# Kernel optimization log

Measured on AMD Instinct MI355X. Metric: run time of the kernel, lower is better.

## Reference

```python
import jax, jax.numpy as jnp
import numpy as np

N_OBJ = 8        # objects per sample -> nc2 = 28 pair-nodes per sample (code caps nc2 < 30)
MAX_REL = 10     # relations per sample (num_rel is uniform so total_rels is static)


def setup_inputs() -> dict:
    key = jax.random.key(0)
    k1, k2, k3, k4, k5 = jax.random.split(key, 5)
    B, D, n = 1024, 512, N_OBJ
    iu, ju = np.triu_indices(n, k=1)                     # (i<j) pair layout, lexicographic
    nc2 = iu.shape[0]                                     # 28
    bcol = np.repeat(np.arange(B), nc2)
    slicing_tensor = jnp.asarray(
        np.stack([bcol, np.tile(iu, B), np.tile(ju, B)], axis=1), dtype=jnp.int32)  # [B*nc2, 3]
    spatial_branch_feature_map = jax.random.normal(k1, (B * nc2, D), dtype=jnp.float32)
    W_self = jax.random.normal(k2, (D, D), dtype=jnp.float32) / np.float32(np.sqrt(D))
    W_nbr = jax.random.normal(k3, (D, D), dtype=jnp.float32) / np.float32(np.sqrt(D))
    b = jnp.zeros((D,), dtype=jnp.float32)
    # object_pairs: distinct indices in [0, n)
    i0 = jax.random.randint(k4, (B, MAX_REL), 0, n)
    off = jax.random.randint(k5, (B, MAX_REL), 1, n)
    i1 = (i0 + off) % n
    object_pairs = jnp.stack([i0, i1], axis=-1).astype(jnp.int32)  # [B, MAX_REL, 2]
    num_rel = jnp.full((B,), MAX_REL, dtype=jnp.int32)
    num_obj = jnp.full((B,), n, dtype=jnp.int32)
    return {"spatial_branch_feature_map": spatial_branch_feature_map, "W_self": W_self,
            "W_nbr": W_nbr, "b": b, "slicing_tensor": slicing_tensor,
            "object_pairs": object_pairs, "num_rel": num_rel, "num_obj": num_obj}


def reference(spatial_branch_feature_map, W_self, W_nbr, b,
              slicing_tensor, object_pairs, num_rel, num_obj):
    x = spatial_branch_feature_map
    N, D = x.shape
    B = num_obj.shape[0]
    nc2 = N // B                                          # pair-nodes per sample
    n = N_OBJ
    # --- fully-connected edge index per sample (incl. self-loops), offset per batch ---
    src_l = jnp.repeat(jnp.arange(nc2, dtype=jnp.int32), nc2)   # row0: t1 outer loop
    dst_l = jnp.tile(jnp.arange(nc2, dtype=jnp.int32), nc2)     # row1: t2 inner loop
    offs = (jnp.arange(B, dtype=jnp.int32) * nc2)[:, None]
    src = (src_l[None, :] + offs).reshape(-1)                   # [B*nc2^2]
    dst = (dst_l[None, :] + offs).reshape(-1)
    # --- GNN layer: sum-aggregate neighbor messages, linear + ReLU ---
    agg = jax.ops.segment_sum(x[src], dst, num_segments=N)      # [N, D]
    h = jax.nn.relu(x @ W_self + agg @ W_nbr + b)               # [N, D]
    # --- key-matching gather (replaces nested python-loop boolean matching) ---
    keys = slicing_tensor[:, 0] * (n * n) + slicing_tensor[:, 1] * n + slicing_tensor[:, 2]
    lut = jnp.zeros((B * n * n,), dtype=jnp.int32).at[keys].set(jnp.arange(N, dtype=jnp.int32))
    pmin = jnp.minimum(object_pairs[..., 0], object_pairs[..., 1])
    pmax = jnp.maximum(object_pairs[..., 0], object_pairs[..., 1])
    bidx = jnp.arange(B, dtype=jnp.int32)[:, None]
    rel_keys = (bidx * (n * n) + pmin * n + pmax).reshape(-1)   # [B*MAX_REL]
    rows = lut[rel_keys]
    return h[rows]                                              # [total_rels, D]
```

## Files before the change

### kernel.cpp

```cpp
#include <hip/hip_runtime.h>
#include <hip/hip_bf16.h>
#include <stdint.h>


typedef __bf16 bf16_t;
typedef __bf16 bf16x8 __attribute__((ext_vector_type(8)));
typedef __bf16 bf16x4 __attribute__((ext_vector_type(4)));
typedef float  f32x4  __attribute__((ext_vector_type(4)));

#define D_DIM 512
#define NC2   28
#define NOBJ  8
#define MAXREL 10
#define B_SAMP 1024
#define OUTROWS (B_SAMP * MAXREL)

__device__ __forceinline__ void gload_lds16(const void* g, void* l) {
  __builtin_amdgcn_global_load_lds(
      (const __attribute__((address_space(1))) unsigned int*)g,
      (__attribute__((address_space(3))) unsigned int*)l, 16, 0, 0);
}

__global__ __launch_bounds__(256) void prep_kernel(
    const float* __restrict__ x, const float* __restrict__ Wself,
    const float* __restrict__ Wnbr, const int* __restrict__ pairs,
    bf16_t* __restrict__ Sbf, bf16_t* __restrict__ Abf,
    bf16_t* __restrict__ Wst, bf16_t* __restrict__ Wnt)
{
  const int blk = blockIdx.x, tid = threadIdx.x;
  if (blk < B_SAMP) {
    __shared__ int rel_row[MAXREL];
    __shared__ float4 oddsum[128];
    if (tid < MAXREL) {
      int p0 = pairs[blk * MAXREL * 2 + tid * 2 + 0];
      int p1 = pairs[blk * MAXREL * 2 + tid * 2 + 1];
      int pmin = min(p0, p1), pmax = max(p0, p1);
      rel_row[tid] = 7 * pmin - (pmin * (pmin - 1)) / 2 + (pmax - pmin - 1);
    }
    __syncthreads();

    const int h = tid >> 7, c = tid & 127;
    const float4* x4 = (const float4*)(x + (size_t)blk * NC2 * D_DIM);
    float4 a = {0.f, 0.f, 0.f, 0.f};
    #pragma unroll
    for (int rp = 0; rp < NC2 / 2; ++rp) {
      float4 v = x4[(rp * 2 + h) * 128 + c];
      a.x += v.x; a.y += v.y; a.z += v.z; a.w += v.w;
    }
    if (h) oddsum[c] = a;
    __syncthreads();
    if (!h) {
      float4 b = oddsum[c];
      bf16x4 o = { (bf16_t)(a.x + b.x), (bf16_t)(a.y + b.y),
                   (bf16_t)(a.z + b.z), (bf16_t)(a.w + b.w) };
      *(bf16x4*)(Sbf + (size_t)blk * D_DIM + c * 4) = o;
    }
    #pragma unroll
    for (int j = h; j < MAXREL; j += 2) {
      float4 v = x4[rel_row[j] * 128 + c];
      bf16x4 o = { (bf16_t)v.x, (bf16_t)v.y, (bf16_t)v.z, (bf16_t)v.w };
      *(bf16x4*)(Abf + (size_t)(blk * MAXREL + j) * D_DIM + c * 4) = o;
    }
  } else {
    __shared__ float tile[32][33];
    const int t = blk - B_SAMP;
    const float* W  = (t & 256) ? Wnbr : Wself;
    bf16_t*     Wt  = (t & 256) ? Wnt  : Wst;
    const int r = t & 255;
    const int k0 = (r & 15) * 32, n0 = (r >> 4) * 32;
    const int tx = tid & 31, ty = tid >> 5;
    #pragma unroll
    for (int i = 0; i < 32; i += 8)
      tile[ty + i][tx] = W[(size_t)(k0 + ty + i) * D_DIM + n0 + tx];
    __syncthreads();
    #pragma unroll
    for (int i = 0; i < 32; i += 8)
      Wt[(size_t)(n0 + ty + i) * D_DIM + k0 + tx] = (bf16_t)tile[tx][ty + i];
  }
}

#define SA_BYTES 6144
#define SB_BYTES 8192
__global__ __launch_bounds__(256, 4) void fused_gemm_kernel(
    const bf16_t* __restrict__ Abf, const bf16_t* __restrict__ Sbf,
    const bf16_t* __restrict__ Wst, const bf16_t* __restrict__ Wnt,
    const float* __restrict__ bias, float* __restrict__ out)
{
  __shared__ __align__(16) unsigned char pool[2 * SA_BYTES + 2 * SB_BYTES];

  const int tid = threadIdx.x;
  const int w = tid >> 6, l = tid & 63;
  const int kg = l >> 4, lr = l & 15;
  const int n0 = blockIdx.y * 64;
  const int n0w = n0 + w * 16;
  const int arow0 = blockIdx.x * 80;
  const int srow0 = blockIdx.x * 8;

  f32x4 acc[6] = {};

  auto STAGE = [&](int bsel, int k0) {
    bf16_t* aB = (bf16_t*)(pool + bsel * SA_BYTES);
    bf16_t* bB = (bf16_t*)(pool + 2 * SA_BYTES + bsel * SB_BYTES);
    #pragma unroll
    for (int r = 0; r < 4; ++r) {
      int slot = r * 4 + w;
      if (slot < 6) {
        int c = slot * 64 + l;
        int row = c >> 2, ch = c & 3;
        int sch = ch ^ ((row >> 1) & 3);
        const bf16_t* g = (slot < 5)
            ? Abf + (size_t)(arow0 + row) * D_DIM + k0 + sch * 8
            : Sbf + (size_t)(srow0 + (row & 7)) * D_DIM + k0 + sch * 8;
        gload_lds16(g, aB + (size_t)slot * 512);
      } else if (slot < 14) {
        int c = (slot - 6) * 64 + l;
        int mat = c >> 8, rc = c & 255;
        int row = rc >> 2, ch = rc & 3;
        int sch = ch ^ ((row >> 1) & 3);
        const bf16_t* W = mat ? Wnt : Wst;
        gload_lds16(W + (size_t)(n0 + row) * D_DIM + k0 + sch * 8,
                    bB + (size_t)(slot - 6) * 512);
      }
    }
  };

  STAGE(0, 0);
  asm volatile("s_waitcnt vmcnt(0)" ::: "memory");
  __builtin_amdgcn_s_barrier();

  const int xorc = (kg ^ ((lr >> 1) & 3)) * 8;
  int cur = 0;
  #pragma unroll
  for (int t = 0; t < 16; ++t) {
    if (t < 15) {
      STAGE(cur ^ 1, (t + 1) * 32);
      if (w < 2) asm volatile("s_waitcnt vmcnt(4)" ::: "memory");
      else       asm volatile("s_waitcnt vmcnt(3)" ::: "memory");
    } else {
      asm volatile("s_waitcnt vmcnt(0)" ::: "memory");
    }
    __builtin_amdgcn_s_barrier();

    const bf16_t* aC = (const bf16_t*)(pool + cur * SA_BYTES);
    const bf16_t* bC = (const bf16_t*)(pool + 2 * SA_BYTES + cur * SB_BYTES);
    bf16x8 af[6], bs, bn;
    #pragma unroll
    for (int s = 0; s < 6; ++s)
      af[s] = *(const bf16x8*)(aC + (s * 16 + lr) * 32 + xorc);
    bs = *(const bf16x8*)(bC + (w * 16 + lr) * 32 + xorc);
    bn = *(const bf16x8*)(bC + 2048 + (w * 16 + lr) * 32 + xorc);

    #pragma unroll
    for (int s = 0; s < 5; ++s)
      acc[s] = __builtin_amdgcn_mfma_f32_16x16x32_bf16(af[s], bs, acc[s], 0, 0, 0);
    acc[5] = __builtin_amdgcn_mfma_f32_16x16x32_bf16(af[5], bn, acc[5], 0, 0, 0);

    __builtin_amdgcn_s_barrier();
    cur ^= 1;
  }

  float* Tex = (float*)pool;
  #pragma unroll
  for (int reg = 0; reg < 4; ++reg)
    Tex[(w * 8 + ((kg * 4 + reg) & 7)) * 20 + lr] = acc[5][reg];
  __syncthreads();

  const float bv = bias[n0w + lr];
  #pragma unroll
  for (int s = 0; s < 5; ++s) {
    #pragma unroll
    for (int reg = 0; reg < 4; ++reg) {
      int rloc = s * 16 + kg * 4 + reg;
      int ls = rloc / MAXREL;
      float v = acc[s][reg] + Tex[(w * 8 + ls) * 20 + lr] + bv;
      out[(size_t)(arow0 + rloc) * D_DIM + n0w + lr] = fmaxf(v, 0.0f);
    }
  }
}

extern "C" void kernel_launch(void* const* d_in, const int* in_sizes, int n_in,
                              void* d_out, int out_size, void* d_ws, size_t ws_size,
                              hipStream_t stream) {
  const float* x     = (const float*)d_in[0];
  const float* Wself = (const float*)d_in[1];
  const float* Wnbr  = (const float*)d_in[2];
  const float* bias  = (const float*)d_in[3];
  const int*   pairs = (const int*)d_in[5];

  char* ws = (char*)d_ws;
  size_t off = 0;
  bf16_t* Sbf = (bf16_t*)(ws + off); off += (size_t)B_SAMP * D_DIM * 2;
  bf16_t* Wst = (bf16_t*)(ws + off); off += (size_t)D_DIM * D_DIM * 2;
  bf16_t* Wnt = (bf16_t*)(ws + off); off += (size_t)D_DIM * D_DIM * 2;
  bf16_t* Abf = (bf16_t*)(ws + off); off += (size_t)OUTROWS * D_DIM * 2;

  prep_kernel<<<B_SAMP + 512, 256, 0, stream>>>(
      x, Wself, Wnbr, pairs, Sbf, Abf, Wst, Wnt);
  fused_gemm_kernel<<<dim3(OUTROWS / 80, D_DIM / 64), 256, 0, stream>>>(
      Abf, Sbf, Wst, Wnt, bias, (float*)d_out);
}
```

Baseline: 36.15 us.

## Load weight operands directly into registers and drop their LDS staging

Result: slower. 40.33 us (+11.6%).

```diff
diff --git a/kernel.cpp b/kernel.cpp
--- a/kernel.cpp
+++ b/kernel.cpp
@@ -80,19 +80,28 @@
 }
 
 #define SA_BYTES 6144
-#define SB_BYTES 8192
-__global__ __launch_bounds__(256, 4) void fused_gemm_kernel(
+
+#define DS_MFMA(AF, BS, BN) do {                                              \
+    _Pragma("unroll")                                                         \
+    for (int s_ = 0; s_ < 6; ++s_)                                            \
+      AF[s_] = *(const bf16x8*)(aC + (s_ * 16 + lr) * 32 + xorc);             \
+    _Pragma("unroll")                                                         \
+    for (int s_ = 0; s_ < 5; ++s_)                                            \
+      acc[s_] = __builtin_amdgcn_mfma_f32_16x16x32_bf16(AF[s_], BS, acc[s_], 0, 0, 0); \
+    acc[5] = __builtin_amdgcn_mfma_f32_16x16x32_bf16(AF[5], BN, acc[5], 0, 0, 0); \
+  } while (0)
+
+__global__ __launch_bounds__(256, 5) void fused_gemm_kernel(
     const bf16_t* __restrict__ Abf, const bf16_t* __restrict__ Sbf,
     const bf16_t* __restrict__ Wst, const bf16_t* __restrict__ Wnt,
     const float* __restrict__ bias, float* __restrict__ out)
 {
-  __shared__ __align__(16) unsigned char pool[2 * SA_BYTES + 2 * SB_BYTES];
+  __shared__ __align__(16) unsigned char pool[2 * SA_BYTES];
 
   const int tid = threadIdx.x;
   const int w = tid >> 6, l = tid & 63;
   const int kg = l >> 4, lr = l & 15;
-  const int n0 = blockIdx.y * 64;
-  const int n0w = n0 + w * 16;
+  const int n0w = blockIdx.y * 64 + w * 16;
   const int arow0 = blockIdx.x * 80;
   const int srow0 = blockIdx.x * 8;
 
@@ -100,61 +109,67 @@
 
   auto STAGE = [&](int bsel, int k0) {
     bf16_t* aB = (bf16_t*)(pool + bsel * SA_BYTES);
-    bf16_t* bB = (bf16_t*)(pool + 2 * SA_BYTES + bsel * SB_BYTES);
-    #pragma unroll
-    for (int r = 0; r < 4; ++r) {
+    #pragma unroll
+    for (int r = 0; r < 2; ++r) {
       int slot = r * 4 + w;
       if (slot < 6) {
         int c = slot * 64 + l;
         int row = c >> 2, ch = c & 3;
         int sch = ch ^ ((row >> 1) & 3);
-        const bf16_t* g = (slot < 5)
+        const bf16_t* g = (row < 80)
             ? Abf + (size_t)(arow0 + row) * D_DIM + k0 + sch * 8
             : Sbf + (size_t)(srow0 + (row & 7)) * D_DIM + k0 + sch * 8;
-        gload_lds16(g, aB + (size_t)slot * 512);
-      } else if (slot < 14) {
-        int c = (slot - 6) * 64 + l;
-        int mat = c >> 8, rc = c & 255;
-        int row = rc >> 2, ch = rc & 3;
-        int sch = ch ^ ((row >> 1) & 3);
-        const bf16_t* W = mat ? Wnt : Wst;
-        gload_lds16(W + (size_t)(n0 + row) * D_DIM + k0 + sch * 8,
-                    bB + (size_t)(slot - 6) * 512);
+        gload_lds16(g, aB + (size_t)c * 8);
       }
     }
   };
 
+  const bf16_t* pBs = Wst + (size_t)(n0w + lr) * D_DIM + kg * 8;
+  const bf16_t* pBn = Wnt + (size_t)(n0w + lr) * D_DIM + kg * 8;
+
+  bf16x8 bsX, bnX, bsY, bnY, af[6];
+
   STAGE(0, 0);
+  bsX = *(const bf16x8*)(pBs);
+  bnX = *(const bf16x8*)(pBn);
   asm volatile("s_waitcnt vmcnt(0)" ::: "memory");
   __builtin_amdgcn_s_barrier();
 
   const int xorc = (kg ^ ((lr >> 1) & 3)) * 8;
   int cur = 0;
   #pragma unroll
-  for (int t = 0; t < 16; ++t) {
-    if (t < 15) {
+  for (int t = 0; t < 16; t += 2) {
+    if (t + 1 < 16) {
       STAGE(cur ^ 1, (t + 1) * 32);
+      bsY = *(const bf16x8*)(pBs + (t + 1) * 32);
+      bnY = *(const bf16x8*)(pBn + (t + 1) * 32);
       if (w < 2) asm volatile("s_waitcnt vmcnt(4)" ::: "memory");
       else       asm volatile("s_waitcnt vmcnt(3)" ::: "memory");
     } else {
       asm volatile("s_waitcnt vmcnt(0)" ::: "memory");
     }
     __builtin_amdgcn_s_barrier();
-
-    const bf16_t* aC = (const bf16_t*)(pool + cur * SA_BYTES);
-    const bf16_t* bC = (const bf16_t*)(pool + 2 * SA_BYTES + cur * SB_BYTES);
-    bf16x8 af[6], bs, bn;
-    #pragma unroll
-    for (int s = 0; s < 6; ++s)
-      af[s] = *(const bf16x8*)(aC + (s * 16 + lr) * 32 + xorc);
-    bs = *(const bf16x8*)(bC + (w * 16 + lr) * 32 + xorc);
-    bn = *(const bf16x8*)(bC + 2048 + (w * 16 + lr) * 32 + xorc);
-
-    #pragma unroll
-    for (int s = 0; s < 5; ++s)
-      acc[s] = __builtin_amdgcn_mfma_f32_16x16x32_bf16(af[s], bs, acc[s], 0, 0, 0);
-    acc[5] = __builtin_amdgcn_mfma_f32_16x16x32_bf16(af[5], bn, acc[5], 0, 0, 0);
-
+    {
+      const bf16_t* aC = (const bf16_t*)(pool + cur * SA_BYTES);
+      DS_MFMA(af, bsX, bnX);
+    }
+    __builtin_amdgcn_s_barrier();
+    cur ^= 1;
+
+    if (t + 2 < 16) {
+      STAGE(cur ^ 1, (t + 2) * 32);
+      bsX = *(const bf16x8*)(pBs + (t + 2) * 32);
+      bnX = *(const bf16x8*)(pBn + (t + 2) * 32);
+      if (w < 2) asm volatile("s_waitcnt vmcnt(4)" ::: "memory");
+      else       asm volatile("s_waitcnt vmcnt(3)" ::: "memory");
+    } else {
+      asm volatile("s_waitcnt vmcnt(0)" ::: "memory");
+    }
+    __builtin_amdgcn_s_barrier();
+    {
+      const bf16_t* aC = (const bf16_t*)(pool + cur * SA_BYTES);
+      DS_MFMA(af, bsY, bnY);
+    }
     __builtin_amdgcn_s_barrier();
     cur ^= 1;
   }
```
